# Performance work log

Hardware: AMD Instinct MI355X
Metric: run time of the kernel (lower is better)

Reference implementation:

```python
import jax, jax.numpy as jnp
import numpy as np

B, S, DIN, DQ, DK = 4, 2048, 1024, 64, 64
NEG_INF = -jnp.inf


def _make_mask(sq, sk):
    # Mirrors createMask: causal mask (-inf where key_idx > query_idx),
    # except 3 randomly chosen (row, col) 'global token' pairs left at 0.
    # torch version uses random.sample; we use a fixed numpy RNG for determinism.
    rng = np.random.default_rng(0)
    g_rows = rng.choice(sk, 3, replace=False)  # sampled from range(lrlen)
    g_cols = rng.choice(sq, 3, replace=False)  # sampled from range(sequence_len)
    row = jnp.arange(sq)[:, None]
    col = jnp.arange(sk)[None, :]
    mask = jnp.where(col > row, NEG_INF, 0.0).astype(jnp.float32)
    mask = mask.at[jnp.asarray(g_rows), jnp.asarray(g_cols)].set(0.0)
    return mask  # [sq, sk]


def setup_inputs() -> dict:
    key = jax.random.key(0)
    ks = jax.random.split(key, 9)
    sc = 1.0 / np.sqrt(DIN)
    return {
        "q": jax.random.normal(ks[0], (B, S, DIN), jnp.float32),
        "k": jax.random.normal(ks[1], (B, S, DIN), jnp.float32),
        "v": jax.random.normal(ks[2], (B, S, DIN), jnp.float32),
        "Wq": jax.random.normal(ks[3], (DIN, DQ), jnp.float32) * sc,
        "bq": jax.random.normal(ks[4], (DQ,), jnp.float32) * sc,
        "Wk": jax.random.normal(ks[5], (DIN, DK), jnp.float32) * sc,
        "bk": jax.random.normal(ks[6], (DK,), jnp.float32) * sc,
        "Wv": jax.random.normal(ks[7], (DIN, DK), jnp.float32) * sc,
        "bv": jax.random.normal(ks[8], (DK,), jnp.float32) * sc,
    }


def reference(q, k, v, Wq, bq, Wk, bk, Wv, bv):
    Q = q @ Wq + bq            # [B,S,DQ]
    K = k @ Wk + bk            # [B,S,DK]
    V = v @ Wv + bv            # [B,S,DK]
    scores = jnp.einsum("bqd,bkd->bqk", Q, K)  # [B,S,S]
    mask = _make_mask(scores.shape[-2], scores.shape[-1])
    denom = jnp.asarray(K.shape[-1], jnp.float32) ** 0.5
    # NOTE: original adds mask BEFORE dividing by sqrt(d_k); -inf survives division.
    attn = jax.nn.softmax((scores + mask) / denom, axis=-1)
    return jnp.einsum("bqk,bkd->bqd", attn, V)  # [B,S,DK]
```

## Files before the change

kernel.cpp:

```cpp
#include <hip/hip_runtime.h>
#include <cstdint>
#include <cstddef>
#include <math.h>

#define SEQ    2048
#define NBATCH 4
#define DIN    1024
#define DH     64

typedef __attribute__((ext_vector_type(8))) short  short8;
typedef __attribute__((ext_vector_type(4))) float  floatx4;

#define MFMA16(a, b, c) __builtin_amdgcn_mfma_f32_16x16x32_bf16((a), (b), (c), 0, 0, 0)

__device__ __forceinline__ unsigned short f2bf(float x) {
  unsigned u = __float_as_uint(x);
  return (unsigned short)((u + 0x8000u) >> 16);
}
__device__ __forceinline__ float bf2f(unsigned short h) {
  return __uint_as_float(((unsigned)h) << 16);
}

__device__ __forceinline__ void async_cp4(const void* g, void* l) {
  __builtin_amdgcn_global_load_lds(
      (const __attribute__((address_space(1))) void*)g,
      (__attribute__((address_space(3))) void*)l, 4, 0, 0);
}

template <int OFF>
__device__ __forceinline__ void gldw(short8 &d, unsigned long long a) {
  asm volatile("global_load_dwordx4 %0, %1, off offset:%2"
               : "=v"(d) : "v"(a), "n"(OFF));
}
#define WAITV(N) asm volatile("s_waitcnt vmcnt(" #N ")" ::: "memory")
#define SB()     __builtin_amdgcn_sched_barrier(0)
#define BAR()    __builtin_amdgcn_s_barrier()

namespace nprng {

struct PCG64 {
  __uint128_t state, inc;
  bool has_uint32;
  uint32_t uinteger;
};

static inline void pcg_step(PCG64 &g) {
  const __uint128_t MULT =
      (((__uint128_t)0x2360ed051fc65da4ULL) << 64) | 0x4385df649fccf645ULL;
  g.state = g.state * MULT + g.inc;
}

static inline uint64_t pcg_output(const PCG64 &g) {
  uint64_t hi = (uint64_t)(g.state >> 64);
  uint64_t lo = (uint64_t)g.state;
  uint64_t x = hi ^ lo;
  unsigned rot = (unsigned)(g.state >> 122) & 63u;
  return (x >> rot) | (x << ((64u - rot) & 63u));
}

static inline uint64_t pcg_next64(PCG64 &g) { pcg_step(g); return pcg_output(g); }

static inline uint32_t pcg_next32(PCG64 &g) {
  if (g.has_uint32) { g.has_uint32 = false; return g.uinteger; }
  uint64_t n = pcg_next64(g);
  g.has_uint32 = true;
  g.uinteger = (uint32_t)(n >> 32);
  return (uint32_t)(n & 0xffffffffu);
}

static inline void pcg_seed_from_seedseq0(PCG64 &g) {
  const uint32_t MULT_A = 0x931e8875u;
  const uint32_t MULT_B = 0x58f38dedu;
  const uint32_t MIX_L  = 0xca01f9ddu;
  const uint32_t MIX_R  = 0x4973f715u;
  uint32_t hc = 0x43b0d7e5u;
  uint32_t pool[4];
  for (int i = 0; i < 4; i++) {
    uint32_t v = 0u;
    v ^= hc; hc *= MULT_A; v *= hc; v ^= v >> 16;
    pool[i] = v;
  }
  for (int is = 0; is < 4; is++) {
    for (int id = 0; id < 4; id++) {
      if (is == id) continue;
      uint32_t h = pool[is];
      h ^= hc; hc *= MULT_A; h *= hc; h ^= h >> 16;
      uint32_t r = (pool[id] * MIX_L) ^ (h * MIX_R);
      r ^= r >> 16;
      pool[id] = r;
    }
  }
  uint32_t hb = 0x8b51f9ddu;
  uint32_t w[8];
  for (int i = 0; i < 8; i++) {
    uint32_t v = pool[i & 3];
    v ^= hb; hb *= MULT_B; v *= hb; v ^= v >> 16;
    w[i] = v;
  }
  uint64_t sv[4];
  for (int k = 0; k < 4; k++)
    sv[k] = (uint64_t)w[2 * k] | ((uint64_t)w[2 * k + 1] << 32);
  __uint128_t initstate = (((__uint128_t)sv[0]) << 64) | sv[1];
  __uint128_t initseq   = (((__uint128_t)sv[2]) << 64) | sv[3];
  g.state = 0; g.inc = (initseq << 1) | 1;
  pcg_step(g);
  g.state += initstate;
  pcg_step(g);
  g.has_uint32 = false; g.uinteger = 0;
}

static inline uint32_t bounded32(PCG64 &g, uint32_t rng ) {
  if (rng == 0) return 0;
  const uint32_t rng_excl = rng + 1u;
  uint64_t m = (uint64_t)pcg_next32(g) * (uint64_t)rng_excl;
  uint32_t leftover = (uint32_t)m;
  if (leftover < rng_excl) {
    const uint32_t threshold = (uint32_t)(0xffffffffu - rng) % rng_excl;
    while (leftover < threshold) {
      m = (uint64_t)pcg_next32(g) * (uint64_t)rng_excl;
      leftover = (uint32_t)m;
    }
  }
  return (uint32_t)(m >> 32);
}

static inline void choice3_2048(PCG64 &g, long long idx[3]) {
  const int pop = 2048, sz = 3;
  uint64_t hs[4] = { (uint64_t)-1, (uint64_t)-1, (uint64_t)-1, (uint64_t)-1 };
  const uint64_t mask = 3;
  for (int j = pop - sz; j < pop; j++) {
    uint64_t val = (uint64_t)bounded32(g, (uint32_t)j);
    uint64_t loc = val & mask;
    while (hs[loc] != (uint64_t)-1 && hs[loc] != val) loc = (loc + 1) & mask;
    if (hs[loc] == (uint64_t)-1) {
      hs[loc] = val;
      idx[j - pop + sz] = (long long)val;
    } else {
      loc = (uint64_t)j & mask;
      while (hs[loc] != (uint64_t)-1) loc = (loc + 1) & mask;
      hs[loc] = (uint64_t)j;
      idx[j - pop + sz] = (long long)j;
    }
  }
  for (int i = 2; i >= 1; i--) {
    uint32_t j = bounded32(g, (uint32_t)i);
    long long t = idx[j]; idx[j] = idx[i]; idx[i] = t;
  }
}

}

__global__ __launch_bounds__(256) void wtrans_kernel(
    const float* __restrict__ Wq, const float* __restrict__ Wk,
    const float* __restrict__ Wv, unsigned short* __restrict__ WTc) {
  const int u = blockIdx.x * 256 + threadIdx.x;
  const int l   = u & 63;
  const int fi  = (u >> 6) & 7;
  const int nch = (u >> 9) & 1;
  const int kc  = (u >> 10) & 7;
  const int p   = u >> 13;
  const int f   = fi & 1;
  const int ks  = fi >> 1;
  const float* W = (p == 0) ? Wq : (p == 1) ? Wk : Wv;
  const int n  = nch * 32 + f * 16 + (l & 15);
  const int k0 = kc * 128 + ks * 32 + ((l >> 4) * 8);
  short8 v;
#pragma unroll
  for (int j = 0; j < 8; j++) v[j] = (short)f2bf(W[(size_t)(k0 + j) * 64 + n]);
  *((short8*)WTc + u) = v;
}

__global__ __launch_bounds__(256, 3) void proj_kernel(
    const float* __restrict__ xq, const float* __restrict__ xk,
    const float* __restrict__ xv, const unsigned short* __restrict__ WTc,
    const float* __restrict__ bq, const float* __restrict__ bk,
    const float* __restrict__ bv,
    unsigned short* __restrict__ Qf, unsigned short* __restrict__ Kf,
    unsigned short* __restrict__ Vf) {
  const int m0g  = blockIdx.x * 32;
  const int proj = m0g >> 13;
  const int m0   = m0g & 8191;
  const float* X    = (proj == 0) ? xq : (proj == 1) ? xk : xv;
  const float* bias = (proj == 0) ? bq : (proj == 1) ? bk : bv;

  const int tid  = threadIdx.x;
  const int w    = tid >> 6;
  const int l    = tid & 63;
  const int quad = l >> 4;
  const int lx   = l & 15;
  const int mr   = (w & 1) * 16;
  const int nc   = (w >> 1) * 32;

  __shared__ __align__(16) char LDSbuf[2 * 16896];

  const float* Xblk = X + (size_t)m0 * DIN;
  const unsigned long long wab =
      (unsigned long long)(const void*)((const short8*)WTc +
                                        ((size_t)(proj * 16 + (w >> 1))) * 512 + l);

  floatx4 acc0 = {0.f, 0.f, 0.f, 0.f}, acc1 = acc0;
  short8  wa[8], wb[8];

#define STAGE(KC, XBUF, WBUF)                                                  \
  {                                                                            \
    float* Xs = (float*)(LDSbuf + (XBUF) * 16896);                             \
    _Pragma("unroll")                                                          \
    for (int i = 0; i < 8; i++) {                                              \
      const int r = 8 * w + i;                                                 \
      const float* g = Xblk + (size_t)r * DIN + (KC) * 128;                    \
      async_cp4(g + l,      &Xs[r * 132]);                                     \
      async_cp4(g + 64 + l, &Xs[r * 132 + 64]);                                \
    }                                                                          \
    const unsigned long long p0 = wab + (KC) * 16384ull;                       \
    const unsigned long long p1 = p0 + 4096ull;                                \
    gldw<   0>(WBUF[0], p0); gldw<1024>(WBUF[1], p0);                          \
    gldw<2048>(WBUF[2], p0); gldw<3072>(WBUF[3], p0);                          \
    gldw<   0>(WBUF[4], p1); gldw<1024>(WBUF[5], p1);                          \
    gldw<2048>(WBUF[6], p1); gldw<3072>(WBUF[7], p1);                          \
  }

#define CONSUME(XBUF, WBUF)                                                    \
  {                                                                            \
    const float* Xs = (const float*)(LDSbuf + (XBUF) * 16896);                 \
    _Pragma("unroll")                                                          \
    for (int ks = 0; ks < 4; ks++) {                                           \
      const float* ap = &Xs[(mr + lx) * 132 + ks * 32 + quad * 8];             \
      const float4 f0 = *(const float4*)ap;                                    \
      const float4 f1 = *(const float4*)(ap + 4);                              \
      short8 a;                                                                \
      a[0] = f2bf(f0.x); a[1] = f2bf(f0.y); a[2] = f2bf(f0.z); a[3] = f2bf(f0.w); \
      a[4] = f2bf(f1.x); a[5] = f2bf(f1.y); a[6] = f2bf(f1.z); a[7] = f2bf(f1.w); \
      acc0 = MFMA16(a, WBUF[2 * ks],     acc0);                                \
      acc1 = MFMA16(a, WBUF[2 * ks + 1], acc1);                                \
    }                                                                          \
  }

  STAGE(0, 0, wa);
  STAGE(1, 1, wb);
  WAITV(24); SB(); BAR(); CONSUME(0, wa); BAR();
  STAGE(2, 0, wa);
  WAITV(24); SB(); BAR(); CONSUME(1, wb); BAR();
  STAGE(3, 1, wb);
  WAITV(24); SB(); BAR(); CONSUME(0, wa); BAR();
  STAGE(4, 0, wa);
  WAITV(24); SB(); BAR(); CONSUME(1, wb); BAR();
  STAGE(5, 1, wb);
  WAITV(24); SB(); BAR(); CONSUME(0, wa); BAR();
  STAGE(6, 0, wa);
  WAITV(24); SB(); BAR(); CONSUME(1, wb); BAR();
  STAGE(7, 1, wb);
  WAITV(24); SB(); BAR(); CONSUME(0, wa); BAR();
  WAITV(0);  SB(); BAR(); CONSUME(1, wb);

#undef STAGE
#undef CONSUME

  float (*Cs)[68] = (float(*)[68])LDSbuf;
  const float bb0 = bias[nc + lx], bb1 = bias[nc + 16 + lx];
#pragma unroll
  for (int i = 0; i < 4; i++) {
    Cs[mr + quad * 4 + i][nc + lx]      = acc0[i] + bb0;
    Cs[mr + quad * 4 + i][nc + 16 + lx] = acc1[i] + bb1;
  }
  __syncthreads();

  const int bq_ = m0 >> 11;
  const int s0  = m0 & 2047;
  if (proj == 0) {
    const int ti = tid >> 7, s = (tid >> 6) & 1, ll = tid & 63;
    const int lxx = ll & 15, qq = ll >> 4;
    short8 v;
#pragma unroll
    for (int j = 0; j < 8; j++) v[j] = (short)f2bf(Cs[ti * 16 + lxx][s * 32 + qq * 8 + j]);
    char* dst = (char*)Qf + ((size_t)(bq_ * 128 + (s0 >> 4) + ti)) * 2048 + s * 1024 + ll * 16;
    *(short8*)dst = v;
  } else if (proj == 1) {
    const int ci = tid >> 7, s = (tid >> 6) & 1, ll = tid & 63;
    const int lxx = ll & 15, qq = ll >> 4;
    const int c = ((s0 >> 4) & 3) + ci;
    short8 v;
#pragma unroll
    for (int j = 0; j < 8; j++) v[j] = (short)f2bf(Cs[ci * 16 + lxx][s * 32 + qq * 8 + j]);
    char* dst = (char*)Kf + ((size_t)(bq_ * 32 + (s0 >> 6))) * 8192 + (c * 2 + s) * 1024 + ll * 16;
    *(short8*)dst = v;
  } else {
    const int c = tid >> 6, ll = tid & 63;
    const int lxx = ll & 15, qq = ll >> 4;
    const int sh = (s0 >> 5) & 1;
    short8 v;
#pragma unroll
    for (int j = 0; j < 8; j++) v[j] = (short)f2bf(Cs[qq * 8 + j][c * 16 + lxx]);
    char* dst = (char*)Vf + ((size_t)(bq_ * 32 + (s0 >> 6))) * 8192 + (sh * 4 + c) * 1024 + ll * 16;
    *(short8*)dst = v;
  }
}

__global__ __launch_bounds__(256, 2) void attn_kernel(
    const unsigned short* __restrict__ Qf, const unsigned short* __restrict__ Kf,
    const unsigned short* __restrict__ Vf, float* __restrict__ out,
    int R0, int C0, int R1, int C1, int R2, int C2) {
  const int b    = blockIdx.y;
  const int bx   = blockIdx.x;
  const int qi   = (bx & 1) ? (127 - (bx >> 1)) : (bx >> 1);
  const int q0   = qi * 16;
  const int tid  = threadIdx.x;
  const int w    = tid >> 6;
  const int l    = tid & 63;
  const int quad = l >> 4;
  const int lx   = l & 15;

  __shared__ unsigned short Ps[4][16][72];
  __shared__ float Os[4][16][64];
  __shared__ float mS[4][16], lS[4][16];
  __shared__ float lgS[3];
  __shared__ int   lgF[3];

  const char* Qc = (const char*)Qf + ((size_t)(b * 128 + qi)) * 2048 + l * 16;
  const short8 aq0 = *(const short8*)Qc;
  const short8 aq1 = *(const short8*)(Qc + 1024);

  floatx4 O[4];
  float m_i[4], l_i[4];
#pragma unroll
  for (int c = 0; c < 4; c++) O[c] = (floatx4){0.f, 0.f, 0.f, 0.f};
#pragma unroll
  for (int i = 0; i < 4; i++) { m_i[i] = -INFINITY; l_i[i] = 0.f; }

  const int T = (q0 + 79) >> 6;

  for (int t = w; t < T; t += 4) {
    const int k0 = t << 6;
    const bool mT = (t == T - 1);

    const char* Kc = (const char*)Kf + ((size_t)(b * 32 + t)) * 8192 + l * 16;
    const char* Vc = (const char*)Vf + ((size_t)(b * 32 + t)) * 8192 + l * 16;
    short8 kf[8], vf[8];
#pragma unroll
    for (int f = 0; f < 8; f++) {
      kf[f] = *(const short8*)(Kc + f * 1024);
      vf[f] = *(const short8*)(Vc + f * 1024);
    }

    floatx4 sc[4];
    __builtin_amdgcn_s_setprio(1);
#pragma unroll
    for (int c = 0; c < 4; c++) {
      sc[c] = (floatx4){0.f, 0.f, 0.f, 0.f};
      sc[c] = MFMA16(aq0, kf[2 * c], sc[c]);
      sc[c] = MFMA16(aq1, kf[2 * c + 1], sc[c]);
    }
    __builtin_amdgcn_s_setprio(0);

    float mt[4], al[4];
#pragma unroll
    for (int i = 0; i < 4; i++) {
      const int rowg = q0 + quad * 4 + i;
      float vmax = -INFINITY;
#pragma unroll
      for (int c = 0; c < 4; c++) {
        float v = sc[c][i] * 0.125f;
        if (mT && (k0 + 16 * c + lx) > rowg) v = -INFINITY;
        sc[c][i] = v;
        vmax = fmaxf(vmax, v);
      }
      mt[i] = vmax;
    }
#pragma unroll
    for (int i = 0; i < 4; i++) {
#pragma unroll
      for (int off = 8; off >= 1; off >>= 1)
        mt[i] = fmaxf(mt[i], __shfl_xor(mt[i], off));
      const float mn = fmaxf(m_i[i], mt[i]);
      al[i] = __expf(m_i[i] - mn);
      m_i[i] = mn;
      float s = 0.f;
#pragma unroll
      for (int c = 0; c < 4; c++) {
        float p = __expf(sc[c][i] - mn);
        Ps[w][quad * 4 + i][16 * c + lx] = f2bf(p);
        s += p;
      }
#pragma unroll
      for (int off = 8; off >= 1; off >>= 1) s += __shfl_xor(s, off);
      l_i[i] = l_i[i] * al[i] + s;
    }
#pragma unroll
    for (int c = 0; c < 4; c++)
#pragma unroll
      for (int i = 0; i < 4; i++) O[c][i] *= al[i];
    asm volatile("" ::: "memory");
    const short8 pf0 = *(const short8*)&Ps[w][lx][quad * 8];
    const short8 pf1 = *(const short8*)&Ps[w][lx][32 + quad * 8];
    __builtin_amdgcn_s_setprio(1);
#pragma unroll
    for (int c = 0; c < 4; c++) {
      O[c] = MFMA16(pf0, vf[c],     O[c]);
      O[c] = MFMA16(pf1, vf[4 + c], O[c]);
    }
    __builtin_amdgcn_s_setprio(0);
  }

  if (lx == 0) {
#pragma unroll
    for (int i = 0; i < 4; i++) {
      mS[w][quad * 4 + i] = m_i[i];
      lS[w][quad * 4 + i] = l_i[i];
    }
  }
#pragma unroll
  for (int c = 0; c < 4; c++)
#pragma unroll
    for (int i = 0; i < 4; i++) Os[w][quad * 4 + i][16 * c + lx] = O[c][i];

  if (w == 0) {
#pragma unroll
    for (int p = 0; p < 3; p++) {
      const int R = (p == 0) ? R0 : (p == 1) ? R1 : R2;
      const int C = (p == 0) ? C0 : (p == 1) ? C1 : C2;
      const int act = (R >= q0 && R < q0 + 16 && C > R);
      float d = 0.f;
      if (act) {
        const int dd = l;
        const char* qa = (const char*)Qf + ((size_t)(b * 128 + (R >> 4))) * 2048 +
                         (dd >> 5) * 1024 + ((R & 15) + ((dd >> 3) & 3) * 16) * 16 + (dd & 7) * 2;
        const char* ka = (const char*)Kf + ((size_t)(b * 32 + (C >> 6))) * 8192 +
                         (((C >> 4) & 3) * 2 + (dd >> 5)) * 1024 +
                         ((C & 15) + ((dd >> 3) & 3) * 16) * 16 + (dd & 7) * 2;
        d = bf2f(*(const unsigned short*)qa) * bf2f(*(const unsigned short*)ka);
#pragma unroll
        for (int off = 32; off >= 1; off >>= 1) d += __shfl_xor(d, off);
        d *= 0.125f;
      }
      if (l == 0) { lgF[p] = act; lgS[p] = d; }
    }
  }
  __syncthreads();

  {
    const int row = tid >> 4;
    const int d0  = (tid & 15) * 4;
    const int Rs[3] = {R0, R1, R2};
    const int Cs3[3] = {C0, C1, C2};

    float mf = -INFINITY;
#pragma unroll
    for (int w4 = 0; w4 < 4; w4++) mf = fmaxf(mf, mS[w4][row]);
#pragma unroll
    for (int p = 0; p < 3; p++)
      if (lgF[p] && (Rs[p] - q0) == row) mf = fmaxf(mf, lgS[p]);

    float lf = 0.f;
    float o0 = 0.f, o1 = 0.f, o2 = 0.f, o3 = 0.f;
#pragma unroll
    for (int w4 = 0; w4 < 4; w4++) {
      const float a = __expf(mS[w4][row] - mf);
      lf += a * lS[w4][row];
      const float* op = &Os[w4][row][d0];
      o0 += a * op[0]; o1 += a * op[1]; o2 += a * op[2]; o3 += a * op[3];
    }
#pragma unroll
    for (int p = 0; p < 3; p++) {
      if (lgF[p] && (Rs[p] - q0) == row) {
        const float pe = __expf(lgS[p] - mf);
        lf += pe;
        const int C = Cs3[p];
        float vv[4];
#pragma unroll
        for (int j = 0; j < 4; j++) {
          const int dim = d0 + j;
          const char* va = (const char*)Vf + ((size_t)(b * 32 + (C >> 6))) * 8192 +
                           (((C >> 5) & 1) * 4 + (dim >> 4)) * 1024 +
                           ((dim & 15) + ((C >> 3) & 3) * 16) * 16 + (C & 7) * 2;
          vv[j] = bf2f(*(const unsigned short*)va);
        }
        o0 += pe * vv[0]; o1 += pe * vv[1]; o2 += pe * vv[2]; o3 += pe * vv[3];
      }
    }
    const float inv = 1.0f / lf;
    float4 r;
    r.x = o0 * inv; r.y = o1 * inv; r.z = o2 * inv; r.w = o3 * inv;
    *(float4*)(out + ((size_t)b * SEQ + q0 + row) * 64 + d0) = r;
  }
}

extern "C" void kernel_launch(void* const* d_in, const int* in_sizes, int n_in,
                              void* d_out, int out_size, void* d_ws,
                              size_t ws_size, hipStream_t stream) {
  const float* xq = (const float*)d_in[0];
  const float* xk = (const float*)d_in[1];
  const float* xv = (const float*)d_in[2];
  const float* Wq = (const float*)d_in[3];
  const float* bq = (const float*)d_in[4];
  const float* Wk = (const float*)d_in[5];
  const float* bk = (const float*)d_in[6];
  const float* Wv = (const float*)d_in[7];
  const float* bv = (const float*)d_in[8];
  float* out = (float*)d_out;

  unsigned short* Qf  = (unsigned short*)d_ws;
  unsigned short* Kf  = Qf + (size_t)NBATCH * SEQ * 64;
  unsigned short* Vf  = Kf + (size_t)NBATCH * SEQ * 64;
  unsigned short* WTc = Vf + (size_t)NBATCH * SEQ * 64;

  nprng::PCG64 g;
  nprng::pcg_seed_from_seedseq0(g);
  long long rows[3], cols[3];
  nprng::choice3_2048(g, rows);
  nprng::choice3_2048(g, cols);

  wtrans_kernel<<<96, 256, 0, stream>>>(Wq, Wk, Wv, WTc);

  proj_kernel<<<768, 256, 0, stream>>>(xq, xk, xv, WTc, bq, bk, bv, Qf, Kf, Vf);

  dim3 agrid(SEQ / 16, NBATCH);
  attn_kernel<<<agrid, 256, 0, stream>>>(
      Qf, Kf, Vf, out, (int)rows[0], (int)cols[0], (int)rows[1], (int)cols[1],
      (int)rows[2], (int)cols[2]);
}
```

Baseline: 155.0 us.

## Use 16-byte async LDS loads with XOR swizzle and triple-buffered X staging

The projection kernel's X tile staging now uses 16-byte global_load_lds transfers instead of 4-byte ones, with an XOR-swizzled LDS layout replacing the padded rows to avoid bank conflicts. X goes through three LDS buffers, so loads run two stages ahead, and the explicit ds_read_b128 reads are issued before the barrier that releases the buffer for refill. The aim is fewer load instructions and better overlap of global memory traffic with MFMA work, at the cost of more LDS use and more intricate wait-count bookkeeping.

Result: no change. 153.0 us (-1.3%).

```diff
diff --git a/kernel.cpp b/kernel.cpp
--- a/kernel.cpp
+++ b/kernel.cpp
@@ -21,10 +21,10 @@
   return __uint_as_float(((unsigned)h) << 16);
 }
 
-__device__ __forceinline__ void async_cp4(const void* g, void* l) {
+__device__ __forceinline__ void async_cp16(const void* g, void* l) {
   __builtin_amdgcn_global_load_lds(
       (const __attribute__((address_space(1))) void*)g,
-      (__attribute__((address_space(3))) void*)l, 4, 0, 0);
+      (__attribute__((address_space(3))) void*)l, 16, 0, 0);
 }
 
 template <int OFF>
@@ -35,6 +35,9 @@
 #define WAITV(N) asm volatile("s_waitcnt vmcnt(" #N ")" ::: "memory")
 #define SB()     __builtin_amdgcn_sched_barrier(0)
 #define BAR()    __builtin_amdgcn_s_barrier()
+
+#define DSR(dst, ra, OFF)                                                      \
+  asm volatile("ds_read_b128 %0, %1 offset:%2" : "=v"(dst) : "v"(ra), "n"(OFF))
 
 namespace nprng {
 
@@ -191,69 +194,80 @@
   const int mr   = (w & 1) * 16;
   const int nc   = (w >> 1) * 32;
 
-  __shared__ __align__(16) char LDSbuf[2 * 16896];
+  __shared__ __align__(16) char LDSbuf[3 * 16384];
 
   const float* Xblk = X + (size_t)m0 * DIN;
+
+  const char *ga0, *ga1, *ga2, *ga3;
+  {
+    const int lh = l >> 5, lu = l & 31;
+#define GAX(i) ((const char*)(Xblk + (size_t)(8 * w + 2 * (i) + lh) * DIN) +    \
+                (size_t)((lu ^ ((2 * (i) + lh) & 7)) << 4))
+    ga0 = GAX(0); ga1 = GAX(1); ga2 = GAX(2); ga3 = GAX(3);
+#undef GAX
+  }
+
+  const unsigned ldsb =
+      (unsigned)(size_t)(__attribute__((address_space(3))) char*)LDSbuf;
+  const unsigned ra0 = ldsb + (mr + lx) * 512 + (((quad * 2 + 0) ^ (lx & 7)) << 4);
+  const unsigned ra1 = ldsb + (mr + lx) * 512 + (((quad * 2 + 1) ^ (lx & 7)) << 4);
+
   const unsigned long long wab =
       (unsigned long long)(const void*)((const short8*)WTc +
                                         ((size_t)(proj * 16 + (w >> 1))) * 512 + l);
 
   floatx4 acc0 = {0.f, 0.f, 0.f, 0.f}, acc1 = acc0;
   short8  wa[8], wb[8];
-
-#define STAGE(KC, XBUF, WBUF)                                                  \
-  {                                                                            \
-    float* Xs = (float*)(LDSbuf + (XBUF) * 16896);                             \
-    _Pragma("unroll")                                                          \
-    for (int i = 0; i < 8; i++) {                                              \
-      const int r = 8 * w + i;                                                 \
-      const float* g = Xblk + (size_t)r * DIN + (KC) * 128;                    \
-      async_cp4(g + l,      &Xs[r * 132]);                                     \
-      async_cp4(g + 64 + l, &Xs[r * 132 + 64]);                                \
-    }                                                                          \
-    const unsigned long long p0 = wab + (KC) * 16384ull;                       \
+  floatx4 x0, x1, x2, x3, x4, x5, x6, x7;
+
+#define STAGEX(KC, XB)                                                         \
+  async_cp16(ga0 + (KC) * 512, LDSbuf + (XB) * 16384 + w * 4096 + 0);          \
+  async_cp16(ga1 + (KC) * 512, LDSbuf + (XB) * 16384 + w * 4096 + 1024);       \
+  async_cp16(ga2 + (KC) * 512, LDSbuf + (XB) * 16384 + w * 4096 + 2048);       \
+  async_cp16(ga3 + (KC) * 512, LDSbuf + (XB) * 16384 + w * 4096 + 3072);
+
+#define STAGEW(KC, WBUF)                                                       \
+  { const unsigned long long p0 = wab + (KC) * 16384ull;                       \
     const unsigned long long p1 = p0 + 4096ull;                                \
     gldw<   0>(WBUF[0], p0); gldw<1024>(WBUF[1], p0);                          \
     gldw<2048>(WBUF[2], p0); gldw<3072>(WBUF[3], p0);                          \
     gldw<   0>(WBUF[4], p1); gldw<1024>(WBUF[5], p1);                          \
-    gldw<2048>(WBUF[6], p1); gldw<3072>(WBUF[7], p1);                          \
-  }
-
-#define CONSUME(XBUF, WBUF)                                                    \
-  {                                                                            \
-    const float* Xs = (const float*)(LDSbuf + (XBUF) * 16896);                 \
-    _Pragma("unroll")                                                          \
-    for (int ks = 0; ks < 4; ks++) {                                           \
-      const float* ap = &Xs[(mr + lx) * 132 + ks * 32 + quad * 8];             \
-      const float4 f0 = *(const float4*)ap;                                    \
-      const float4 f1 = *(const float4*)(ap + 4);                              \
-      short8 a;                                                                \
-      a[0] = f2bf(f0.x); a[1] = f2bf(f0.y); a[2] = f2bf(f0.z); a[3] = f2bf(f0.w); \
-      a[4] = f2bf(f1.x); a[5] = f2bf(f1.y); a[6] = f2bf(f1.z); a[7] = f2bf(f1.w); \
-      acc0 = MFMA16(a, WBUF[2 * ks],     acc0);                                \
-      acc1 = MFMA16(a, WBUF[2 * ks + 1], acc1);                                \
-    }                                                                          \
-  }
-
-  STAGE(0, 0, wa);
-  STAGE(1, 1, wb);
-  WAITV(24); SB(); BAR(); CONSUME(0, wa); BAR();
-  STAGE(2, 0, wa);
-  WAITV(24); SB(); BAR(); CONSUME(1, wb); BAR();
-  STAGE(3, 1, wb);
-  WAITV(24); SB(); BAR(); CONSUME(0, wa); BAR();
-  STAGE(4, 0, wa);
-  WAITV(24); SB(); BAR(); CONSUME(1, wb); BAR();
-  STAGE(5, 1, wb);
-  WAITV(24); SB(); BAR(); CONSUME(0, wa); BAR();
-  STAGE(6, 0, wa);
-  WAITV(24); SB(); BAR(); CONSUME(1, wb); BAR();
-  STAGE(7, 1, wb);
-  WAITV(24); SB(); BAR(); CONSUME(0, wa); BAR();
-  WAITV(0);  SB(); BAR(); CONSUME(1, wb);
-
-#undef STAGE
-#undef CONSUME
+    gldw<2048>(WBUF[6], p1); gldw<3072>(WBUF[7], p1); }
+
+#define READX(XB)                                                              \
+  DSR(x0, ra0, (XB) * 16384 + 0);   DSR(x1, ra1, (XB) * 16384 + 0);            \
+  DSR(x2, ra0, (XB) * 16384 + 128); DSR(x3, ra1, (XB) * 16384 + 128);          \
+  DSR(x4, ra0, (XB) * 16384 + 256); DSR(x5, ra1, (XB) * 16384 + 256);          \
+  DSR(x6, ra0, (XB) * 16384 + 384); DSR(x7, ra1, (XB) * 16384 + 384);          \
+  asm volatile("s_waitcnt lgkmcnt(0)" ::: "memory");                           \
+  __builtin_amdgcn_sched_barrier(0);
+
+#define CVTM(f0, f1, w0, w1)                                                   \
+  { short8 a_;                                                                 \
+    a_[0] = f2bf(f0[0]); a_[1] = f2bf(f0[1]); a_[2] = f2bf(f0[2]); a_[3] = f2bf(f0[3]); \
+    a_[4] = f2bf(f1[0]); a_[5] = f2bf(f1[1]); a_[6] = f2bf(f1[2]); a_[7] = f2bf(f1[3]); \
+    acc0 = MFMA16(a_, w0, acc0); acc1 = MFMA16(a_, w1, acc1); }
+
+#define DOMFMA(WBUF)                                                           \
+  CVTM(x0, x1, WBUF[0], WBUF[1]); CVTM(x2, x3, WBUF[2], WBUF[3]);              \
+  CVTM(x4, x5, WBUF[4], WBUF[5]); CVTM(x6, x7, WBUF[6], WBUF[7]);
+
+  STAGEX(0, 0); STAGEW(0, wa); STAGEX(1, 1); STAGEW(1, wb); STAGEX(2, 2);
+
+  WAITV(16); SB(); BAR(); READX(0); BAR(); DOMFMA(wa); STAGEW(2, wa); STAGEX(3, 0);
+  WAITV(16); SB(); BAR(); READX(1); BAR(); DOMFMA(wb); STAGEW(3, wb); STAGEX(4, 1);
+  WAITV(16); SB(); BAR(); READX(2); BAR(); DOMFMA(wa); STAGEW(4, wa); STAGEX(5, 2);
+  WAITV(16); SB(); BAR(); READX(0); BAR(); DOMFMA(wb); STAGEW(5, wb); STAGEX(6, 0);
+  WAITV(16); SB(); BAR(); READX(1); BAR(); DOMFMA(wa); STAGEW(6, wa); STAGEX(7, 1);
+  WAITV(16); SB(); BAR(); READX(2); BAR(); DOMFMA(wb); STAGEW(7, wb);
+  WAITV(12); SB(); BAR(); READX(0); BAR(); DOMFMA(wa);
+  WAITV(0);  SB(); BAR(); READX(1); BAR(); DOMFMA(wb);
+
+#undef STAGEX
+#undef STAGEW
+#undef READX
+#undef CVTM
+#undef DOMFMA
 
   float (*Cs)[68] = (float(*)[68])LDSbuf;
   const float bb0 = bias[nc + lx], bb1 = bias[nc + 16 + lx];
```
